# Performance work log

Hardware: AMD Instinct MI355X
Metric: run time of the kernel (lower is better)

## Reference

```python
import jax, jax.numpy as jnp
import numpy as np

DIM = 1024
HEADS = 16
DIM_HEAD = 64
INNER = HEADS * DIM_HEAD
EPS = 1e-5


def layernorm(x, g, b):
    mu = jnp.mean(x, axis=-1, keepdims=True)
    var = jnp.mean((x - mu) ** 2, axis=-1, keepdims=True)
    return (x - mu) * jax.lax.rsqrt(var + EPS) * g + b


def setup_inputs() -> dict:
    key = jax.random.key(0)
    ks = jax.random.split(key, 8)
    B, S = 2, 2048
    s_in = (2.0 / DIM) ** 0.5
    return {
        "x": jax.random.normal(ks[0], (B, S, DIM), jnp.float32),
        "w_qkv": jax.random.normal(ks[1], (DIM, 3 * INNER), jnp.float32) * s_in,
        "w_out": jax.random.normal(ks[2], (INNER, DIM), jnp.float32) * s_in,
        "b_out": jnp.zeros((DIM,), jnp.float32),
        "g1": jnp.ones((DIM,), jnp.float32),
        "beta1": jnp.zeros((DIM,), jnp.float32),
        "g2": jnp.ones((DIM,), jnp.float32),
        "beta2": jnp.zeros((DIM,), jnp.float32),
        "w_ff1": jax.random.normal(ks[3], (DIM, 4 * DIM), jnp.float32) * s_in,
        "b_ff1": jnp.zeros((4 * DIM,), jnp.float32),
        "w_ff2": jax.random.normal(ks[4], (4 * DIM, DIM), jnp.float32) * (2.0 / (4 * DIM)) ** 0.5,
        "b_ff2": jnp.zeros((DIM,), jnp.float32),
    }


def reference(x, w_qkv, w_out, b_out, g1, beta1, g2, beta2, w_ff1, b_ff1, w_ff2, b_ff2):
    B, S, D = x.shape
    scale = DIM_HEAD ** -0.5
    # --- attention block (pre-norm) ---
    h = layernorm(x, g1, beta1)
    qkv = h @ w_qkv  # [B,S,3*INNER]
    q, k, v = jnp.split(qkv, 3, axis=-1)
    def heads(t):
        return t.reshape(B, S, HEADS, DIM_HEAD).transpose(0, 2, 1, 3)  # [B,H,S,dh]
    q, k, v = heads(q), heads(k), heads(v)
    attn = jnp.einsum("bhsd,bhtd->bhst", q, k) * scale
    attn = jax.nn.softmax(attn, axis=-1)
    out = jnp.einsum("bhst,bhtd->bhsd", attn, v)
    out = out.transpose(0, 2, 1, 3).reshape(B, S, INNER)
    x = x + out @ w_out + b_out
    # --- FFN block (pre-norm) ---
    h = layernorm(x, g2, beta2)
    h = jax.nn.gelu(h @ w_ff1 + b_ff1, approximate=False)
    x = x + h @ w_ff2 + b_ff2
    return x
```

## Files before the change

### kernel.cpp

```cpp
#include <hip/hip_runtime.h>
#include <math.h>

typedef unsigned short u16;
typedef __attribute__((ext_vector_type(4))) float f32x4;
typedef __attribute__((ext_vector_type(16))) float f32x16;
typedef __attribute__((ext_vector_type(4))) unsigned short u16x4;
typedef __attribute__((ext_vector_type(8))) __bf16 bf16x8;

static constexpr int SS   = 2048;
static constexpr int DD   = 1024;
static constexpr int HH   = 16;
static constexpr int DH   = 64;
static constexpr int NTOK = 4096;
static constexpr int NQKV = 3072;

#define DEV static __device__ __forceinline__
#define GLD_AS1(p) ((__attribute__((address_space(1))) void*)(void*)(p))
#define GLD_AS3(p) ((__attribute__((address_space(3))) void*)(p))

DEV u16 f2bf(float f) {
    union { float f; unsigned int i; } v; v.f = f;
    unsigned int r = v.i + 0x7fffu + ((v.i >> 16) & 1u);
    return (u16)(r >> 16);
}

DEV f32x4 MFMA(bf16x8 a, bf16x8 b, f32x4 c) {
    return __builtin_amdgcn_mfma_f32_16x16x32_bf16(a, b, c, 0, 0, 0);
}
DEV f32x16 MFMA32(bf16x8 a, bf16x8 b, f32x16 c) {
    return __builtin_amdgcn_mfma_f32_32x32x16_bf16(a, b, c, 0, 0, 0);
}
DEV f32x16 zero16() {
    f32x16 z;
    #pragma unroll
    for (int i = 0; i < 16; i++) z[i] = 0.f;
    return z;
}

__global__ __launch_bounds__(256)
void k_transpose(const float* __restrict__ in, u16* __restrict__ out, int R, int C) {
    __shared__ float tile[32][33];
    int c0 = blockIdx.x * 32, r0 = blockIdx.y * 32;
    int tx = threadIdx.x, ty = threadIdx.y;
    #pragma unroll
    for (int i = 0; i < 32; i += 8)
        tile[ty + i][tx] = in[(size_t)(r0 + ty + i) * C + c0 + tx];
    __syncthreads();
    #pragma unroll
    for (int i = 0; i < 32; i += 8)
        out[(size_t)(c0 + ty + i) * R + r0 + tx] = f2bf(tile[tx][ty + i]);
}

__global__ __launch_bounds__(256)
void k_layernorm(const float* __restrict__ x, const float* __restrict__ g,
                 const float* __restrict__ b, u16* __restrict__ out) {
    int row = blockIdx.x, t = threadIdx.x;
    const float4* xp = reinterpret_cast<const float4*>(x + (size_t)row * DD);
    float4 v = xp[t];
    float s = v.x + v.y + v.z + v.w;
    float q = v.x * v.x + v.y * v.y + v.z * v.z + v.w * v.w;
    #pragma unroll
    for (int m = 1; m < 64; m <<= 1) { s += __shfl_xor(s, m); q += __shfl_xor(q, m); }
    __shared__ float ps[4], pq[4];
    int w = t >> 6, l = t & 63;
    if (l == 0) { ps[w] = s; pq[w] = q; }
    __syncthreads();
    s = ps[0] + ps[1] + ps[2] + ps[3];
    q = pq[0] + pq[1] + pq[2] + pq[3];
    float mu = s * (1.0f / DD);
    float var = q * (1.0f / DD) - mu * mu;
    float rstd = rsqrtf(var + 1e-5f);
    float4 gv = reinterpret_cast<const float4*>(g)[t];
    float4 bv = reinterpret_cast<const float4*>(b)[t];
    u16x4 o;
    o.x = f2bf((v.x - mu) * rstd * gv.x + bv.x);
    o.y = f2bf((v.y - mu) * rstd * gv.y + bv.y);
    o.z = f2bf((v.z - mu) * rstd * gv.z + bv.z);
    o.w = f2bf((v.w - mu) * rstd * gv.w + bv.w);
    reinterpret_cast<u16x4*>(out + (size_t)row * DD)[t] = o;
}

template<int MODE>
__global__ __launch_bounds__(256)
void k_gemm(const u16* __restrict__ A, const u16* __restrict__ BT,
            float* __restrict__ Cf, u16* __restrict__ Cb,
            const float* __restrict__ bias, const float* __restrict__ res,
            u16* __restrict__ vT, int M, int N, int K) {
    __shared__ __align__(128) char lds[2][32768];
    const int t = threadIdx.x;
    const int w = t >> 6, l = t & 63;
    const int lg = l >> 4, lr = l & 15;
    const int m0 = blockIdx.y * 128, n0 = blockIdx.x * 128;
    const int wr = w >> 1, wc = w & 1;

    const int csw = ((l & 7) ^ (l >> 3)) << 3;
    const int chunk0 = w * 4;
    const int srow = (l >> 3);

    f32x4 acc[4][4];
    #pragma unroll
    for (int i = 0; i < 4; i++)
        #pragma unroll
        for (int j = 0; j < 4; j++)
            acc[i][j] = (f32x4){0.f, 0.f, 0.f, 0.f};

    #pragma unroll
    for (int i = 0; i < 4; i++) {
        const int chunk = chunk0 + i;
        const int r = chunk * 8 + srow;
        __builtin_amdgcn_global_load_lds(GLD_AS1(A  + (size_t)(m0 + r) * K + csw),
                                         GLD_AS3(lds[0] + chunk * 1024), 16, 0, 0);
        __builtin_amdgcn_global_load_lds(GLD_AS1(BT + (size_t)(n0 + r) * K + csw),
                                         GLD_AS3(lds[0] + 16384 + chunk * 1024), 16, 0, 0);
    }
    __syncthreads();

    int buf = 0;
    for (int kt = 0; kt < K; kt += 64) {
        if (kt + 64 < K) {
            #pragma unroll
            for (int i = 0; i < 4; i++) {
                const int chunk = chunk0 + i;
                const int r = chunk * 8 + srow;
                __builtin_amdgcn_global_load_lds(GLD_AS1(A  + (size_t)(m0 + r) * K + kt + 64 + csw),
                                                 GLD_AS3(lds[buf ^ 1] + chunk * 1024), 16, 0, 0);
                __builtin_amdgcn_global_load_lds(GLD_AS1(BT + (size_t)(n0 + r) * K + kt + 64 + csw),
                                                 GLD_AS3(lds[buf ^ 1] + 16384 + chunk * 1024), 16, 0, 0);
            }
        }
        const char* Al = lds[buf];
        const char* Bl = lds[buf] + 16384;
        #pragma unroll
        for (int s = 0; s < 2; s++) {
            const int swz = (s * 64 + lg * 16) ^ ((lr & 7) << 4);
            bf16x8 af[4], bfr[4];
            #pragma unroll
            for (int mi = 0; mi < 4; mi++)
                af[mi] = *reinterpret_cast<const bf16x8*>(Al + (wr * 64 + mi * 16 + lr) * 128 + swz);
            #pragma unroll
            for (int ni = 0; ni < 4; ni++)
                bfr[ni] = *reinterpret_cast<const bf16x8*>(Bl + (wc * 64 + ni * 16 + lr) * 128 + swz);
            #pragma unroll
            for (int mi = 0; mi < 4; mi++)
                #pragma unroll
                for (int ni = 0; ni < 4; ni++)
                    acc[mi][ni] = MFMA(af[mi], bfr[ni], acc[mi][ni]);
        }
        __syncthreads();
        buf ^= 1;
    }

    #pragma unroll
    for (int mi = 0; mi < 4; mi++) {
        #pragma unroll
        for (int ni = 0; ni < 4; ni++) {
            int nn = n0 + wc * 64 + ni * 16 + lr;
            #pragma unroll
            for (int r = 0; r < 4; r++) {
                int mm = m0 + wr * 64 + mi * 16 + lg * 4 + r;
                float v = acc[mi][ni][r];
                if (MODE == 0) {
                    if (nn < 2048) {
                        Cb[(size_t)mm * NQKV + nn] = f2bf(v);
                    } else {
                        int b = mm >> 11, sIdx = mm & 2047;
                        int hd = nn - 2048;
                        vT[(((size_t)(b * HH + (hd >> 6)) * DH) + (hd & 63)) * SS + sIdx] = f2bf(v);
                    }
                } else if (MODE == 1) {
                    Cf[(size_t)mm * N + nn] = v + bias[nn] + res[(size_t)mm * N + nn];
                } else {
                    float u = v + bias[nn];
                    float gl = 0.5f * u * (1.0f + erff(u * 0.70710678118654752f));
                    Cb[(size_t)mm * N + nn] = f2bf(gl);
                }
            }
        }
    }
}

__global__ __launch_bounds__(256)
void k_attn(const u16* __restrict__ qkv, const u16* __restrict__ vT,
            u16* __restrict__ out) {
    const int w = threadIdx.x >> 6, l = threadIdx.x & 63;
    const int q = l & 31, hi = l >> 5;
    const int task = (blockIdx.x & 7) * 64 + (blockIdx.x >> 3);
    const int bh = task >> 4;
    const int qg = task & 15;
    const int b = bh >> 4, h = bh & 15;
    const size_t rowbase = (size_t)b * SS;
    const int q0 = (qg * 4 + w) * 32;

    __shared__ __align__(128) u16 Kl[2][32 * 64];
    __shared__ __align__(128) u16 Vl[2][32 * 64];

    const u16* kbase = qkv + rowbase * NQKV + 1024 + h * DH;
    const u16* vbase = vT + (size_t)bh * DH * SS;

    const int srow = w * 8 + (l >> 3);
    const int sslot = (l & 7) ^ (l >> 3);
    const u16* kg = kbase + (size_t)srow * NQKV + sslot * 8;
    const u16* vg = vbase + (size_t)(srow + 32 * (sslot >> 2)) * SS + (sslot & 3) * 8;

    const u16* qrow = qkv + (rowbase + q0 + q) * NQKV + h * DH + hi * 8;
    bf16x8 qf[4];
    #pragma unroll
    for (int ks = 0; ks < 4; ks++)
        qf[ks] = *reinterpret_cast<const bf16x8*>(qrow + ks * 16);

    f32x16 o0 = zero16(), o1 = zero16();
    float mQ = -1e30f, lQ = 0.f;

    __builtin_amdgcn_global_load_lds(GLD_AS1(kg), GLD_AS3((u16*)Kl[0] + w * 512), 16, 0, 0);
    __builtin_amdgcn_global_load_lds(GLD_AS1(vg), GLD_AS3((u16*)Vl[0] + w * 512), 16, 0, 0);
    __syncthreads();

    int buf = 0;
    for (int kv0 = 0; kv0 < SS; kv0 += 32) {
        if (kv0 + 32 < SS) {
            __builtin_amdgcn_global_load_lds(GLD_AS1(kg + (size_t)(kv0 + 32) * NQKV),
                                             GLD_AS3((u16*)Kl[buf ^ 1] + w * 512), 16, 0, 0);
            __builtin_amdgcn_global_load_lds(GLD_AS1(vg + (kv0 + 32)),
                                             GLD_AS3((u16*)Vl[buf ^ 1] + w * 512), 16, 0, 0);
        }
        const u16* Kb = Kl[buf];
        const u16* Vb = Vl[buf];
        const int qsw = (q & 7) << 3;

        f32x16 st = zero16();
        #pragma unroll
        for (int ks = 0; ks < 4; ks++) {
            bf16x8 kf = *reinterpret_cast<const bf16x8*>(Kb + q * 64 + ((ks * 16 + hi * 8) ^ qsw));
            st = MFMA32(kf, qf[ks], st);
        }

        f32x16 sc = st * 0.125f;
        float tm = sc[0];
        #pragma unroll
        for (int i = 1; i < 16; i++) tm = fmaxf(tm, sc[i]);
        tm = fmaxf(tm, __shfl_xor(tm, 32));

        if (!__all(tm - mQ <= 8.f)) {
            float mn = fmaxf(mQ, tm);
            float scale = __expf(mQ - mn);
            lQ *= scale;
            o0 *= scale;
            o1 *= scale;
            mQ = mn;
        }

        f32x16 p;
        #pragma unroll
        for (int i = 0; i < 16; i++) p[i] = __expf(sc[i] - mQ);
        float ts = p[0];
        #pragma unroll
        for (int i = 1; i < 16; i++) ts += p[i];
        ts += __shfl_xor(ts, 32);
        lQ += ts;

        union W { unsigned int u; __bf16 h[2]; };
        W pw[8];
        #pragma unroll
        for (int m = 0; m < 8; m++) {
            pw[m].h[0] = (__bf16)p[2 * m];
            pw[m].h[1] = (__bf16)p[2 * m + 1];
        }

        bf16x8 pf[2];
        #pragma unroll
        for (int kk = 0; kk < 2; kk++) {
            unsigned int a0 = pw[4 * kk + 0].u, a1 = pw[4 * kk + 1].u;
            unsigned int b0 = pw[4 * kk + 2].u, b1 = pw[4 * kk + 3].u;
            unsigned int own0 = hi ? b0 : a0, own1 = hi ? b1 : a1;
            unsigned int snd0 = hi ? a0 : b0, snd1 = hi ? a1 : b1;
            unsigned int r0 = __shfl_xor(snd0, 32), r1 = __shfl_xor(snd1, 32);
            union F { unsigned int u[4]; bf16x8 v; } f;
            f.u[0] = hi ? r0 : own0;
            f.u[1] = hi ? r1 : own1;
            f.u[2] = hi ? own0 : r0;
            f.u[3] = hi ? own1 : r1;
            pf[kk] = f.v;
        }

        #pragma unroll
        for (int kk = 0; kk < 2; kk++) {
            bf16x8 v0 = *reinterpret_cast<const bf16x8*>(Vb + q * 64 + ((kk * 16 + hi * 8) ^ qsw));
            bf16x8 v1 = *reinterpret_cast<const bf16x8*>(Vb + q * 64 + ((32 + kk * 16 + hi * 8) ^ qsw));
            o0 = MFMA32(v0, pf[kk], o0);
            o1 = MFMA32(v1, pf[kk], o1);
        }

        __syncthreads();
        buf ^= 1;
    }

    float invl = 1.0f / lQ;
    u16* orow = out + (rowbase + q0 + q) * DD + h * DH + hi * 4;
    #pragma unroll
    for (int a = 0; a < 4; a++) {
        u16x4 s0v, s1v;
        #pragma unroll
        for (int i = 0; i < 4; i++) {
            s0v[i] = f2bf(o0[4 * a + i] * invl);
            s1v[i] = f2bf(o1[4 * a + i] * invl);
        }
        *reinterpret_cast<u16x4*>(orow + 8 * a)      = s0v;
        *reinterpret_cast<u16x4*>(orow + 32 + 8 * a) = s1v;
    }
}

extern "C" void kernel_launch(void* const* d_in, const int* in_sizes, int n_in,
                              void* d_out, int out_size, void* d_ws, size_t ws_size,
                              hipStream_t stream) {
    (void)in_sizes; (void)n_in; (void)out_size; (void)ws_size;
    const float* x     = (const float*)d_in[0];
    const float* w_qkv = (const float*)d_in[1];
    const float* w_out = (const float*)d_in[2];
    const float* b_out = (const float*)d_in[3];
    const float* g1    = (const float*)d_in[4];
    const float* be1   = (const float*)d_in[5];
    const float* g2    = (const float*)d_in[6];
    const float* be2   = (const float*)d_in[7];
    const float* w_ff1 = (const float*)d_in[8];
    const float* b_ff1 = (const float*)d_in[9];
    const float* w_ff2 = (const float*)d_in[10];
    const float* b_ff2 = (const float*)d_in[11];

    char* ws = (char*)d_ws;
    u16*   W  = (u16*)(ws);
    u16*   Hb = (u16*)(ws + 8388608);
    u16*   QF = (u16*)(ws + 16777216);
    u16*   VT = (u16*)(ws + 50331648);
    u16*   AO = (u16*)(ws + 58720256);
    float* X1 = (float*)(ws + 67108864);
    float* OUT = (float*)d_out;

    k_layernorm<<<NTOK, 256, 0, stream>>>(x, g1, be1, Hb);
    k_transpose<<<dim3(3072 / 32, 1024 / 32), dim3(32, 8), 0, stream>>>(w_qkv, W, 1024, 3072);
    k_gemm<0><<<dim3(3072 / 128, 4096 / 128), 256, 0, stream>>>(
        Hb, W, nullptr, QF, nullptr, nullptr, VT, NTOK, NQKV, 1024);
    k_attn<<<512, 256, 0, stream>>>(QF, VT, AO);
    k_transpose<<<dim3(1024 / 32, 1024 / 32), dim3(32, 8), 0, stream>>>(w_out, W, 1024, 1024);
    k_gemm<1><<<dim3(1024 / 128, 4096 / 128), 256, 0, stream>>>(
        AO, W, X1, nullptr, b_out, x, nullptr, NTOK, 1024, 1024);
    k_layernorm<<<NTOK, 256, 0, stream>>>(X1, g2, be2, Hb);
    k_transpose<<<dim3(4096 / 32, 1024 / 32), dim3(32, 8), 0, stream>>>(w_ff1, W, 1024, 4096);
    k_gemm<2><<<dim3(4096 / 128, 4096 / 128), 256, 0, stream>>>(
        Hb, W, nullptr, QF, b_ff1, nullptr, nullptr, NTOK, 4096, 1024);
    k_transpose<<<dim3(1024 / 32, 4096 / 32), dim3(32, 8), 0, stream>>>(w_ff2, W, 4096, 1024);
    k_gemm<1><<<dim3(1024 / 128, 4096 / 128), 256, 0, stream>>>(
        QF, W, OUT, nullptr, b_ff2, X1, nullptr, NTOK, 1024, 4096);
}
```

Baseline: 290.4 us.

## Split attention KV range across wave pairs and split-K the FFN2 GEMM

Attention now assigns two waves per query tile, each covering half of the KV sequence. The two partial softmax states are merged through LDS at the end, and the grid doubles to 1024 blocks. Exp is rewritten as exp2 with a pre-scaled log2e factor. The final FFN GEMM (K=4096) is split into two K halves with bf16 partial outputs, followed by a new reduce kernel that adds the residual and bias. This is meant to raise parallelism and occupancy, at the cost of bf16 rounding of the partial sums and an extra launch plus memory pass.

```diff
diff --git a/kernel.cpp b/kernel.cpp
--- a/kernel.cpp
+++ b/kernel.cpp
@@ -22,6 +22,9 @@
     union { float f; unsigned int i; } v; v.f = f;
     unsigned int r = v.i + 0x7fffu + ((v.i >> 16) & 1u);
     return (u16)(r >> 16);
+}
+DEV float bdec(u16 u) {
+    union { unsigned int i; float f; } v; v.i = ((unsigned int)u) << 16; return v.f;
 }
 
 DEV f32x4 MFMA(bf16x8 a, bf16x8 b, f32x4 c) {
@@ -93,6 +96,13 @@
     const int m0 = blockIdx.y * 128, n0 = blockIdx.x * 128;
     const int wr = w >> 1, wc = w & 1;
 
+    int kbeg = 0, kend = K;
+    if (MODE == 3) {
+        const int kh = K >> 1;
+        kbeg = blockIdx.z * kh;
+        kend = kbeg + kh;
+    }
+
     const int csw = ((l & 7) ^ (l >> 3)) << 3;
     const int chunk0 = w * 4;
     const int srow = (l >> 3);
@@ -108,16 +118,16 @@
     for (int i = 0; i < 4; i++) {
         const int chunk = chunk0 + i;
         const int r = chunk * 8 + srow;
-        __builtin_amdgcn_global_load_lds(GLD_AS1(A  + (size_t)(m0 + r) * K + csw),
+        __builtin_amdgcn_global_load_lds(GLD_AS1(A  + (size_t)(m0 + r) * K + kbeg + csw),
                                          GLD_AS3(lds[0] + chunk * 1024), 16, 0, 0);
-        __builtin_amdgcn_global_load_lds(GLD_AS1(BT + (size_t)(n0 + r) * K + csw),
+        __builtin_amdgcn_global_load_lds(GLD_AS1(BT + (size_t)(n0 + r) * K + kbeg + csw),
                                          GLD_AS3(lds[0] + 16384 + chunk * 1024), 16, 0, 0);
     }
     __syncthreads();
 
     int buf = 0;
-    for (int kt = 0; kt < K; kt += 64) {
-        if (kt + 64 < K) {
+    for (int kt = kbeg; kt < kend; kt += 64) {
+        if (kt + 64 < kend) {
             #pragma unroll
             for (int i = 0; i < 4; i++) {
                 const int chunk = chunk0 + i;
@@ -169,14 +179,34 @@
                     }
                 } else if (MODE == 1) {
                     Cf[(size_t)mm * N + nn] = v + bias[nn] + res[(size_t)mm * N + nn];
-                } else {
+                } else if (MODE == 2) {
                     float u = v + bias[nn];
                     float gl = 0.5f * u * (1.0f + erff(u * 0.70710678118654752f));
                     Cb[(size_t)mm * N + nn] = f2bf(gl);
+                } else {
+                    u16* dst = blockIdx.z ? vT : Cb;
+                    dst[(size_t)mm * N + nn] = f2bf(v);
                 }
             }
         }
     }
+}
+
+__global__ __launch_bounds__(256)
+void k_ffreduce(const float* __restrict__ X1, const u16* __restrict__ P0,
+                const u16* __restrict__ P1, const float* __restrict__ bias,
+                float* __restrict__ OUT) {
+    int i = blockIdx.x * 256 + threadIdx.x;
+    float4 xv = reinterpret_cast<const float4*>(X1)[i];
+    u16x4 a = reinterpret_cast<const u16x4*>(P0)[i];
+    u16x4 b = reinterpret_cast<const u16x4*>(P1)[i];
+    float4 bv = reinterpret_cast<const float4*>(bias)[i & (DD / 4 - 1)];
+    float4 o;
+    o.x = xv.x + bdec(a.x) + bdec(b.x) + bv.x;
+    o.y = xv.y + bdec(a.y) + bdec(b.y) + bv.y;
+    o.z = xv.z + bdec(a.z) + bdec(b.z) + bv.z;
+    o.w = xv.w + bdec(a.w) + bdec(b.w) + bv.w;
+    reinterpret_cast<float4*>(OUT)[i] = o;
 }
 
 __global__ __launch_bounds__(256)
@@ -184,23 +214,29 @@
             u16* __restrict__ out) {
     const int w = threadIdx.x >> 6, l = threadIdx.x & 63;
     const int q = l & 31, hi = l >> 5;
-    const int task = (blockIdx.x & 7) * 64 + (blockIdx.x >> 3);
-    const int bh = task >> 4;
-    const int qg = task & 15;
+    const int wq = w & 1, wh = w >> 1;
+    const int task = (blockIdx.x & 7) * 128 + (blockIdx.x >> 3);
+    const int bh = task >> 5;
+    const int qpair = task & 31;
     const int b = bh >> 4, h = bh & 15;
     const size_t rowbase = (size_t)b * SS;
-    const int q0 = (qg * 4 + w) * 32;
-
-    __shared__ __align__(128) u16 Kl[2][32 * 64];
-    __shared__ __align__(128) u16 Vl[2][32 * 64];
+    const int q0 = (qpair * 2 + wq) * 32;
+
+    __shared__ __align__(128) u16 Kst[2][2][32 * 64];
+    __shared__ __align__(128) u16 Vst[2][2][32 * 64];
+    __shared__ float ml[4][32][2];
 
     const u16* kbase = qkv + rowbase * NQKV + 1024 + h * DH;
     const u16* vbase = vT + (size_t)bh * DH * SS;
 
-    const int srow = w * 8 + (l >> 3);
     const int sslot = (l & 7) ^ (l >> 3);
-    const u16* kg = kbase + (size_t)srow * NQKV + sslot * 8;
-    const u16* vg = vbase + (size_t)(srow + 32 * (sslot >> 2)) * SS + (sslot & 3) * 8;
+    const int r0i = 16 * wq + (l >> 3);
+    const int kvoff = wh * 1024;
+    const u16* kg0 = kbase + (size_t)(kvoff + r0i) * NQKV + sslot * 8;
+    const u16* kg1 = kg0 + (size_t)8 * NQKV;
+    const u16* vg0 = vbase + (size_t)(r0i + 32 * (sslot >> 2)) * SS + kvoff + (sslot & 3) * 8;
+    const u16* vg1 = vg0 + (size_t)8 * SS;
+    const int ch0 = (2 * wq) * 512, ch1 = (2 * wq + 1) * 512;
 
     const u16* qrow = qkv + (rowbase + q0 + q) * NQKV + h * DH + hi * 8;
     bf16x8 qf[4];
@@ -209,22 +245,29 @@
         qf[ks] = *reinterpret_cast<const bf16x8*>(qrow + ks * 16);
 
     f32x16 o0 = zero16(), o1 = zero16();
-    float mQ = -1e30f, lQ = 0.f;
-
-    __builtin_amdgcn_global_load_lds(GLD_AS1(kg), GLD_AS3((u16*)Kl[0] + w * 512), 16, 0, 0);
-    __builtin_amdgcn_global_load_lds(GLD_AS1(vg), GLD_AS3((u16*)Vl[0] + w * 512), 16, 0, 0);
+    float m2 = -1e30f, lQ = 0.f;
+    const float C2 = 0.18033688011112042f;
+
+    __builtin_amdgcn_global_load_lds(GLD_AS1(kg0), GLD_AS3(&Kst[0][wh][ch0]), 16, 0, 0);
+    __builtin_amdgcn_global_load_lds(GLD_AS1(kg1), GLD_AS3(&Kst[0][wh][ch1]), 16, 0, 0);
+    __builtin_amdgcn_global_load_lds(GLD_AS1(vg0), GLD_AS3(&Vst[0][wh][ch0]), 16, 0, 0);
+    __builtin_amdgcn_global_load_lds(GLD_AS1(vg1), GLD_AS3(&Vst[0][wh][ch1]), 16, 0, 0);
     __syncthreads();
 
     int buf = 0;
-    for (int kv0 = 0; kv0 < SS; kv0 += 32) {
-        if (kv0 + 32 < SS) {
-            __builtin_amdgcn_global_load_lds(GLD_AS1(kg + (size_t)(kv0 + 32) * NQKV),
-                                             GLD_AS3((u16*)Kl[buf ^ 1] + w * 512), 16, 0, 0);
-            __builtin_amdgcn_global_load_lds(GLD_AS1(vg + (kv0 + 32)),
-                                             GLD_AS3((u16*)Vl[buf ^ 1] + w * 512), 16, 0, 0);
-        }
-        const u16* Kb = Kl[buf];
-        const u16* Vb = Vl[buf];
+    for (int kv0 = 0; kv0 < 1024; kv0 += 32) {
+        if (kv0 + 32 < 1024) {
+            __builtin_amdgcn_global_load_lds(GLD_AS1(kg0 + (size_t)(kv0 + 32) * NQKV),
+                                             GLD_AS3(&Kst[buf ^ 1][wh][ch0]), 16, 0, 0);
+            __builtin_amdgcn_global_load_lds(GLD_AS1(kg1 + (size_t)(kv0 + 32) * NQKV),
+                                             GLD_AS3(&Kst[buf ^ 1][wh][ch1]), 16, 0, 0);
+            __builtin_amdgcn_global_load_lds(GLD_AS1(vg0 + (kv0 + 32)),
+                                             GLD_AS3(&Vst[buf ^ 1][wh][ch0]), 16, 0, 0);
+            __builtin_amdgcn_global_load_lds(GLD_AS1(vg1 + (kv0 + 32)),
+                                             GLD_AS3(&Vst[buf ^ 1][wh][ch1]), 16, 0, 0);
+        }
+        const u16* Kb = Kst[buf][wh];
+        const u16* Vb = Vst[buf][wh];
         const int qsw = (q & 7) << 3;
 
         f32x16 st = zero16();
@@ -234,24 +277,26 @@
             st = MFMA32(kf, qf[ks], st);
         }
 
-        f32x16 sc = st * 0.125f;
-        float tm = sc[0];
-        #pragma unroll
-        for (int i = 1; i < 16; i++) tm = fmaxf(tm, sc[i]);
+        f32x16 sc = st * C2;
+        float tm = fmaxf(fmaxf(sc[0], sc[1]), fmaxf(sc[2], sc[3]));
+        float tm1 = fmaxf(fmaxf(sc[4], sc[5]), fmaxf(sc[6], sc[7]));
+        float tm2 = fmaxf(fmaxf(sc[8], sc[9]), fmaxf(sc[10], sc[11]));
+        float tm3 = fmaxf(fmaxf(sc[12], sc[13]), fmaxf(sc[14], sc[15]));
+        tm = fmaxf(fmaxf(tm, tm1), fmaxf(tm2, tm3));
         tm = fmaxf(tm, __shfl_xor(tm, 32));
 
-        if (!__all(tm - mQ <= 8.f)) {
-            float mn = fmaxf(mQ, tm);
-            float scale = __expf(mQ - mn);
+        if (!__all(tm - m2 <= 11.5416f)) {
+            float mn = fmaxf(m2, tm);
+            float scale = exp2f(m2 - mn);
             lQ *= scale;
             o0 *= scale;
             o1 *= scale;
-            mQ = mn;
+            m2 = mn;
         }
 
         f32x16 p;
         #pragma unroll
-        for (int i = 0; i < 16; i++) p[i] = __expf(sc[i] - mQ);
+        for (int i = 0; i < 16; i++) p[i] = exp2f(sc[i] - m2);
         float ts = p[0];
         #pragma unroll
         for (int i = 1; i < 16; i++) ts += p[i];
@@ -294,18 +339,48 @@
         buf ^= 1;
     }
 
-    float invl = 1.0f / lQ;
-    u16* orow = out + (rowbase + q0 + q) * DD + h * DH + hi * 4;
-    #pragma unroll
-    for (int a = 0; a < 4; a++) {
-        u16x4 s0v, s1v;
-        #pragma unroll
-        for (int i = 0; i < 4; i++) {
-            s0v[i] = f2bf(o0[4 * a + i] * invl);
-            s1v[i] = f2bf(o1[4 * a + i] * invl);
-        }
-        *reinterpret_cast<u16x4*>(orow + 8 * a)      = s0v;
-        *reinterpret_cast<u16x4*>(orow + 32 + 8 * a) = s1v;
+    f32x4* obuf = reinterpret_cast<f32x4*>(&Kst[0][0][0]);
+    if (hi == 0) { ml[w][q][0] = m2; ml[w][q][1] = lQ; }
+    __syncthreads();
+    const int pw2 = w ^ 2;
+    const float mO = ml[pw2][q][0];
+    const float lO = ml[pw2][q][1];
+    const float mT = fmaxf(m2, mO);
+    const float myS = exp2f(m2 - mT);
+    lQ *= myS;
+    o0 *= myS;
+    o1 *= myS;
+    if (wh) {
+        union U { f32x16 v; f32x4 s[4]; } u0, u1;
+        u0.v = o0; u1.v = o1;
+        #pragma unroll
+        for (int j = 0; j < 4; j++) obuf[(wq * 64 + l) * 8 + (j ^ (l & 7))] = u0.s[j];
+        #pragma unroll
+        for (int j = 0; j < 4; j++) obuf[(wq * 64 + l) * 8 + ((4 + j) ^ (l & 7))] = u1.s[j];
+    }
+    __syncthreads();
+    if (!wh) {
+        const float lT = lQ + lO * exp2f(mO - mT);
+        const float invl = 1.0f / lT;
+        union U { f32x16 v; f32x4 s[4]; } u0, u1;
+        #pragma unroll
+        for (int j = 0; j < 4; j++) u0.s[j] = obuf[(wq * 64 + l) * 8 + (j ^ (l & 7))];
+        #pragma unroll
+        for (int j = 0; j < 4; j++) u1.s[j] = obuf[(wq * 64 + l) * 8 + ((4 + j) ^ (l & 7))];
+        o0 += u0.v;
+        o1 += u1.v;
+        u16* orow = out + (rowbase + q0 + q) * DD + h * DH + hi * 4;
+        #pragma unroll
+        for (int a = 0; a < 4; a++) {
+            u16x4 s0v, s1v;
+            #pragma unroll
+            for (int i = 0; i < 4; i++) {
+                s0v[i] = f2bf(o0[4 * a + i] * invl);
+                s1v[i] = f2bf(o1[4 * a + i] * invl);
+            }
+            *reinterpret_cast<u16x4*>(orow + 8 * a)      = s0v;
+            *reinterpret_cast<u16x4*>(orow + 32 + 8 * a) = s1v;
+        }
     }
 }
 
@@ -339,7 +414,7 @@
     k_transpose<<<dim3(3072 / 32, 1024 / 32), dim3(32, 8), 0, stream>>>(w_qkv, W, 1024, 3072);
     k_gemm<0><<<dim3(3072 / 128, 4096 / 128), 256, 0, stream>>>(
         Hb, W, nullptr, QF, nullptr, nullptr, VT, NTOK, NQKV, 1024);
-    k_attn<<<512, 256, 0, stream>>>(QF, VT, AO);
+    k_attn<<<1024, 256, 0, stream>>>(QF, VT, AO);
     k_transpose<<<dim3(1024 / 32, 1024 / 32), dim3(32, 8), 0, stream>>>(w_out, W, 1024, 1024);
     k_gemm<1><<<dim3(1024 / 128, 4096 / 128), 256, 0, stream>>>(
         AO, W, X1, nullptr, b_out, x, nullptr, NTOK, 1024, 1024);
@@ -348,6 +423,7 @@
     k_gemm<2><<<dim3(4096 / 128, 4096 / 128), 256, 0, stream>>>(
         Hb, W, nullptr, QF, b_ff1, nullptr, nullptr, NTOK, 4096, 1024);
     k_transpose<<<dim3(1024 / 32, 4096 / 32), dim3(32, 8), 0, stream>>>(w_ff2, W, 4096, 1024);
-    k_gemm<1><<<dim3(1024 / 128, 4096 / 128), 256, 0, stream>>>(
-        QF, W, OUT, nullptr, b_ff2, X1, nullptr, NTOK, 1024, 4096);
-}
+    k_gemm<3><<<dim3(1024 / 128, 4096 / 128, 2), 256, 0, stream>>>(
+        QF, W, nullptr, VT, nullptr, nullptr, AO, NTOK, 1024, 4096);
+    k_ffreduce<<<NTOK * DD / 4 / 256, 256, 0, stream>>>(X1, VT, AO, b_ff2, OUT);
+}
```

Measured after the change: 304.9 us. 5.0% more time.

## Split-K the N=1024 GEMMs and widen attention KV tiles to 64

Applied to the files above, without the earlier changes.

The two output-projection GEMMs with N=1024 now use a two-way split-K over blockIdx.z. This doubles the block count from 256 to 512 so more of the GPU's compute units have work. Each half writes bf16 partials, and a new elementwise kernel adds them together with the bias and residual in fp32. Separately, the attention kernel processes 64 keys per iteration instead of 32 and uses exp2 with a folded log2e scale, which halves the loop and barrier count. The trade-offs are extra partial-sum traffic, a bf16 rounding of the partials, and a larger LDS footprint for attention.

```diff
diff --git a/kernel.cpp b/kernel.cpp
--- a/kernel.cpp
+++ b/kernel.cpp
@@ -22,6 +22,9 @@
     union { float f; unsigned int i; } v; v.f = f;
     unsigned int r = v.i + 0x7fffu + ((v.i >> 16) & 1u);
     return (u16)(r >> 16);
+}
+DEV float bdec(u16 u) {
+    union { unsigned int i; float f; } v; v.i = ((unsigned int)u) << 16; return v.f;
 }
 
 DEV f32x4 MFMA(bf16x8 a, bf16x8 b, f32x4 c) {
@@ -93,6 +96,13 @@
     const int m0 = blockIdx.y * 128, n0 = blockIdx.x * 128;
     const int wr = w >> 1, wc = w & 1;
 
+    int kbeg = 0, kend = K;
+    if (MODE == 3) {
+        const int kh = K >> 1;
+        kbeg = blockIdx.z * kh;
+        kend = kbeg + kh;
+    }
+
     const int csw = ((l & 7) ^ (l >> 3)) << 3;
     const int chunk0 = w * 4;
     const int srow = (l >> 3);
@@ -108,16 +118,16 @@
     for (int i = 0; i < 4; i++) {
         const int chunk = chunk0 + i;
         const int r = chunk * 8 + srow;
-        __builtin_amdgcn_global_load_lds(GLD_AS1(A  + (size_t)(m0 + r) * K + csw),
+        __builtin_amdgcn_global_load_lds(GLD_AS1(A  + (size_t)(m0 + r) * K + kbeg + csw),
                                          GLD_AS3(lds[0] + chunk * 1024), 16, 0, 0);
-        __builtin_amdgcn_global_load_lds(GLD_AS1(BT + (size_t)(n0 + r) * K + csw),
+        __builtin_amdgcn_global_load_lds(GLD_AS1(BT + (size_t)(n0 + r) * K + kbeg + csw),
                                          GLD_AS3(lds[0] + 16384 + chunk * 1024), 16, 0, 0);
     }
     __syncthreads();
 
     int buf = 0;
-    for (int kt = 0; kt < K; kt += 64) {
-        if (kt + 64 < K) {
+    for (int kt = kbeg; kt < kend; kt += 64) {
+        if (kt + 64 < kend) {
             #pragma unroll
             for (int i = 0; i < 4; i++) {
                 const int chunk = chunk0 + i;
@@ -167,16 +177,34 @@
                         int hd = nn - 2048;
                         vT[(((size_t)(b * HH + (hd >> 6)) * DH) + (hd & 63)) * SS + sIdx] = f2bf(v);
                     }
-                } else if (MODE == 1) {
-                    Cf[(size_t)mm * N + nn] = v + bias[nn] + res[(size_t)mm * N + nn];
-                } else {
+                } else if (MODE == 2) {
                     float u = v + bias[nn];
                     float gl = 0.5f * u * (1.0f + erff(u * 0.70710678118654752f));
                     Cb[(size_t)mm * N + nn] = f2bf(gl);
+                } else {
+                    u16* dst = blockIdx.z ? vT : Cb;
+                    dst[(size_t)mm * N + nn] = f2bf(v);
                 }
             }
         }
     }
+}
+
+__global__ __launch_bounds__(256)
+void k_ffreduce(const float* __restrict__ RES, const u16* __restrict__ P0,
+                const u16* __restrict__ P1, const float* __restrict__ bias,
+                float* __restrict__ OUT) {
+    int i = blockIdx.x * 256 + threadIdx.x;
+    float4 xv = reinterpret_cast<const float4*>(RES)[i];
+    u16x4 a = reinterpret_cast<const u16x4*>(P0)[i];
+    u16x4 b = reinterpret_cast<const u16x4*>(P1)[i];
+    float4 bv = reinterpret_cast<const float4*>(bias)[i & (DD / 4 - 1)];
+    float4 o;
+    o.x = xv.x + bdec(a.x) + bdec(b.x) + bv.x;
+    o.y = xv.y + bdec(a.y) + bdec(b.y) + bv.y;
+    o.z = xv.z + bdec(a.z) + bdec(b.z) + bv.z;
+    o.w = xv.w + bdec(a.w) + bdec(b.w) + bv.w;
+    reinterpret_cast<float4*>(OUT)[i] = o;
 }
 
 __global__ __launch_bounds__(256)
@@ -191,16 +219,20 @@
     const size_t rowbase = (size_t)b * SS;
     const int q0 = (qg * 4 + w) * 32;
 
-    __shared__ __align__(128) u16 Kl[2][32 * 64];
-    __shared__ __align__(128) u16 Vl[2][32 * 64];
+    __shared__ __align__(128) u16 Kl[2][64 * 64];
+    __shared__ __align__(128) u16 Vl[2][64 * 64];
 
     const u16* kbase = qkv + rowbase * NQKV + 1024 + h * DH;
     const u16* vbase = vT + (size_t)bh * DH * SS;
 
-    const int srow = w * 8 + (l >> 3);
-    const int sslot = (l & 7) ^ (l >> 3);
-    const u16* kg = kbase + (size_t)srow * NQKV + sslot * 8;
-    const u16* vg = vbase + (size_t)(srow + 32 * (sslot >> 2)) * SS + (sslot & 3) * 8;
+    const int srow8 = l >> 3;
+    const int sslot = (l & 7) ^ srow8;
+    const int kr0 = w * 8 + srow8;
+    const u16* kg0 = kbase + (size_t)kr0 * NQKV + sslot * 8;
+    const u16* kg1 = kbase + (size_t)(kr0 + 32) * NQKV + sslot * 8;
+    const u16* vg0 = vbase + (size_t)kr0 * SS + sslot * 8;
+    const u16* vg1 = vbase + (size_t)(kr0 + 32) * SS + sslot * 8;
+    const int chA = (w * 8) * 64, chB = (w * 8 + 32) * 64;
 
     const u16* qrow = qkv + (rowbase + q0 + q) * NQKV + h * DH + hi * 8;
     bf16x8 qf[4];
@@ -209,68 +241,92 @@
         qf[ks] = *reinterpret_cast<const bf16x8*>(qrow + ks * 16);
 
     f32x16 o0 = zero16(), o1 = zero16();
-    float mQ = -1e30f, lQ = 0.f;
-
-    __builtin_amdgcn_global_load_lds(GLD_AS1(kg), GLD_AS3((u16*)Kl[0] + w * 512), 16, 0, 0);
-    __builtin_amdgcn_global_load_lds(GLD_AS1(vg), GLD_AS3((u16*)Vl[0] + w * 512), 16, 0, 0);
+    float m2 = -1e30f, lQ = 0.f;
+    const float C2 = 0.18033688011112042f;
+
+    __builtin_amdgcn_global_load_lds(GLD_AS1(kg0), GLD_AS3((u16*)Kl[0] + chA), 16, 0, 0);
+    __builtin_amdgcn_global_load_lds(GLD_AS1(kg1), GLD_AS3((u16*)Kl[0] + chB), 16, 0, 0);
+    __builtin_amdgcn_global_load_lds(GLD_AS1(vg0), GLD_AS3((u16*)Vl[0] + chA), 16, 0, 0);
+    __builtin_amdgcn_global_load_lds(GLD_AS1(vg1), GLD_AS3((u16*)Vl[0] + chB), 16, 0, 0);
     __syncthreads();
 
     int buf = 0;
-    for (int kv0 = 0; kv0 < SS; kv0 += 32) {
-        if (kv0 + 32 < SS) {
-            __builtin_amdgcn_global_load_lds(GLD_AS1(kg + (size_t)(kv0 + 32) * NQKV),
-                                             GLD_AS3((u16*)Kl[buf ^ 1] + w * 512), 16, 0, 0);
-            __builtin_amdgcn_global_load_lds(GLD_AS1(vg + (kv0 + 32)),
-                                             GLD_AS3((u16*)Vl[buf ^ 1] + w * 512), 16, 0, 0);
+    for (int kv0 = 0; kv0 < SS; kv0 += 64) {
+        if (kv0 + 64 < SS) {
+            __builtin_amdgcn_global_load_lds(GLD_AS1(kg0 + (size_t)(kv0 + 64) * NQKV),
+                                             GLD_AS3((u16*)Kl[buf ^ 1] + chA), 16, 0, 0);
+            __builtin_amdgcn_global_load_lds(GLD_AS1(kg1 + (size_t)(kv0 + 64) * NQKV),
+                                             GLD_AS3((u16*)Kl[buf ^ 1] + chB), 16, 0, 0);
+            __builtin_amdgcn_global_load_lds(GLD_AS1(vg0 + (kv0 + 64)),
+                                             GLD_AS3((u16*)Vl[buf ^ 1] + chA), 16, 0, 0);
+            __builtin_amdgcn_global_load_lds(GLD_AS1(vg1 + (kv0 + 64)),
+                                             GLD_AS3((u16*)Vl[buf ^ 1] + chB), 16, 0, 0);
         }
         const u16* Kb = Kl[buf];
         const u16* Vb = Vl[buf];
         const int qsw = (q & 7) << 3;
 
-        f32x16 st = zero16();
+        f32x16 st0 = zero16(), st1 = zero16();
         #pragma unroll
         for (int ks = 0; ks < 4; ks++) {
-            bf16x8 kf = *reinterpret_cast<const bf16x8*>(Kb + q * 64 + ((ks * 16 + hi * 8) ^ qsw));
-            st = MFMA32(kf, qf[ks], st);
-        }
-
-        f32x16 sc = st * 0.125f;
-        float tm = sc[0];
-        #pragma unroll
-        for (int i = 1; i < 16; i++) tm = fmaxf(tm, sc[i]);
+            const int off = (ks * 16 + hi * 8) ^ qsw;
+            bf16x8 kf0 = *reinterpret_cast<const bf16x8*>(Kb + q * 64 + off);
+            bf16x8 kf1 = *reinterpret_cast<const bf16x8*>(Kb + (q + 32) * 64 + off);
+            st0 = MFMA32(kf0, qf[ks], st0);
+            st1 = MFMA32(kf1, qf[ks], st1);
+        }
+
+        f32x16 sc0 = st0 * C2, sc1 = st1 * C2;
+        float ta = fmaxf(fmaxf(sc0[0], sc0[1]), fmaxf(sc0[2], sc0[3]));
+        float tb = fmaxf(fmaxf(sc0[4], sc0[5]), fmaxf(sc0[6], sc0[7]));
+        float tc = fmaxf(fmaxf(sc0[8], sc0[9]), fmaxf(sc0[10], sc0[11]));
+        float td = fmaxf(fmaxf(sc0[12], sc0[13]), fmaxf(sc0[14], sc0[15]));
+        float te = fmaxf(fmaxf(sc1[0], sc1[1]), fmaxf(sc1[2], sc1[3]));
+        float tf = fmaxf(fmaxf(sc1[4], sc1[5]), fmaxf(sc1[6], sc1[7]));
+        float tg = fmaxf(fmaxf(sc1[8], sc1[9]), fmaxf(sc1[10], sc1[11]));
+        float th = fmaxf(fmaxf(sc1[12], sc1[13]), fmaxf(sc1[14], sc1[15]));
+        float tm = fmaxf(fmaxf(fmaxf(ta, tb), fmaxf(tc, td)),
+                         fmaxf(fmaxf(te, tf), fmaxf(tg, th)));
         tm = fmaxf(tm, __shfl_xor(tm, 32));
 
-        if (!__all(tm - mQ <= 8.f)) {
-            float mn = fmaxf(mQ, tm);
-            float scale = __expf(mQ - mn);
+        if (!__all(tm - m2 <= 11.5416f)) {
+            float mn = fmaxf(m2, tm);
+            float scale = exp2f(m2 - mn);
             lQ *= scale;
             o0 *= scale;
             o1 *= scale;
-            mQ = mn;
-        }
-
-        f32x16 p;
-        #pragma unroll
-        for (int i = 0; i < 16; i++) p[i] = __expf(sc[i] - mQ);
-        float ts = p[0];
-        #pragma unroll
-        for (int i = 1; i < 16; i++) ts += p[i];
+            m2 = mn;
+        }
+
+        f32x16 p0, p1;
+        #pragma unroll
+        for (int i = 0; i < 16; i++) p0[i] = exp2f(sc0[i] - m2);
+        #pragma unroll
+        for (int i = 0; i < 16; i++) p1[i] = exp2f(sc1[i] - m2);
+        float ts = p0[0];
+        #pragma unroll
+        for (int i = 1; i < 16; i++) ts += p0[i];
+        #pragma unroll
+        for (int i = 0; i < 16; i++) ts += p1[i];
         ts += __shfl_xor(ts, 32);
         lQ += ts;
 
         union W { unsigned int u; __bf16 h[2]; };
-        W pw[8];
+        W pw[16];
         #pragma unroll
         for (int m = 0; m < 8; m++) {
-            pw[m].h[0] = (__bf16)p[2 * m];
-            pw[m].h[1] = (__bf16)p[2 * m + 1];
-        }
-
-        bf16x8 pf[2];
-        #pragma unroll
-        for (int kk = 0; kk < 2; kk++) {
-            unsigned int a0 = pw[4 * kk + 0].u, a1 = pw[4 * kk + 1].u;
-            unsigned int b0 = pw[4 * kk + 2].u, b1 = pw[4 * kk + 3].u;
+            pw[m].h[0] = (__bf16)p0[2 * m];
+            pw[m].h[1] = (__bf16)p0[2 * m + 1];
+            pw[8 + m].h[0] = (__bf16)p1[2 * m];
+            pw[8 + m].h[1] = (__bf16)p1[2 * m + 1];
+        }
+
+        bf16x8 pf[4];
+        #pragma unroll
+        for (int kk = 0; kk < 4; kk++) {
+            const int base = (kk >> 1) * 8 + (kk & 1) * 4;
+            unsigned int a0 = pw[base + 0].u, a1 = pw[base + 1].u;
+            unsigned int b0 = pw[base + 2].u, b1 = pw[base + 3].u;
             unsigned int own0 = hi ? b0 : a0, own1 = hi ? b1 : a1;
             unsigned int snd0 = hi ? a0 : b0, snd1 = hi ? a1 : b1;
             unsigned int r0 = __shfl_xor(snd0, 32), r1 = __shfl_xor(snd1, 32);
@@ -283,9 +339,10 @@
         }
 
         #pragma unroll
-        for (int kk = 0; kk < 2; kk++) {
-            bf16x8 v0 = *reinterpret_cast<const bf16x8*>(Vb + q * 64 + ((kk * 16 + hi * 8) ^ qsw));
-            bf16x8 v1 = *reinterpret_cast<const bf16x8*>(Vb + q * 64 + ((32 + kk * 16 + hi * 8) ^ qsw));
+        for (int kk = 0; kk < 4; kk++) {
+            const int off = (kk * 16 + hi * 8) ^ qsw;
+            bf16x8 v0 = *reinterpret_cast<const bf16x8*>(Vb + q * 64 + off);
+            bf16x8 v1 = *reinterpret_cast<const bf16x8*>(Vb + (q + 32) * 64 + off);
             o0 = MFMA32(v0, pf[kk], o0);
             o1 = MFMA32(v1, pf[kk], o1);
         }
@@ -341,13 +398,15 @@
         Hb, W, nullptr, QF, nullptr, nullptr, VT, NTOK, NQKV, 1024);
     k_attn<<<512, 256, 0, stream>>>(QF, VT, AO);
     k_transpose<<<dim3(1024 / 32, 1024 / 32), dim3(32, 8), 0, stream>>>(w_out, W, 1024, 1024);
-    k_gemm<1><<<dim3(1024 / 128, 4096 / 128), 256, 0, stream>>>(
-        AO, W, X1, nullptr, b_out, x, nullptr, NTOK, 1024, 1024);
+    k_gemm<3><<<dim3(1024 / 128, 4096 / 128, 2), 256, 0, stream>>>(
+        AO, W, nullptr, Hb, nullptr, nullptr, VT, NTOK, 1024, 1024);
+    k_ffreduce<<<NTOK * DD / 4 / 256, 256, 0, stream>>>(x, Hb, VT, b_out, X1);
     k_layernorm<<<NTOK, 256, 0, stream>>>(X1, g2, be2, Hb);
     k_transpose<<<dim3(4096 / 32, 1024 / 32), dim3(32, 8), 0, stream>>>(w_ff1, W, 1024, 4096);
     k_gemm<2><<<dim3(4096 / 128, 4096 / 128), 256, 0, stream>>>(
         Hb, W, nullptr, QF, b_ff1, nullptr, nullptr, NTOK, 4096, 1024);
     k_transpose<<<dim3(1024 / 32, 4096 / 32), dim3(32, 8), 0, stream>>>(w_ff2, W, 4096, 1024);
-    k_gemm<1><<<dim3(1024 / 128, 4096 / 128), 256, 0, stream>>>(
-        QF, W, OUT, nullptr, b_ff2, X1, nullptr, NTOK, 1024, 4096);
-}
+    k_gemm<3><<<dim3(1024 / 128, 4096 / 128, 2), 256, 0, stream>>>(
+        QF, W, nullptr, VT, nullptr, nullptr, AO, NTOK, 1024, 4096);
+    k_ffreduce<<<NTOK * DD / 4 / 256, 256, 0, stream>>>(X1, VT, AO, b_ff2, OUT);
+}
```

Measured after the change: 294.9 us. Within noise of the previous version (+1.6%).
